# Performance work log

Measured on AMD Instinct MI355X. Metric: run time of the kernel, lower is better.

## Reference

```python
import jax, jax.numpy as jnp
import numpy as np

B, C, L = 16, 384, 4096
KS, NS = 32, 6
KLEN = KS * 2 ** (NS - 1)  # 1024, must be < L
DECAY = 2.0  # multiplier = linspace(2,2,C) == 2 everywhere
EPS = 1e-5


def setup_inputs() -> dict:
    key = jax.random.key(0)
    ks = jax.random.split(key, 10)
    x = jax.random.normal(ks[0], (B, C, L), jnp.float32)
    t_cond = jax.random.normal(ks[1], (B, C // 3, L), jnp.float32)
    # SLConv params (heads=1): per-scale kernels (NS, heads=1, C, KS) and skip D (1, C)
    kernels = jax.random.normal(ks[2], (NS, 1, C, KS), jnp.float32)
    D = jax.random.normal(ks[3], (1, C), jnp.float32)
    # adaLN linear: Linear(C//3 -> 6C). Original zero-inits (identity block); use small random.
    ada_w = jax.random.normal(ks[4], (6 * C, C // 3), jnp.float32) * 0.02
    ada_b = jax.random.normal(ks[5], (6 * C,), jnp.float32) * 0.02
    # 1x1 conv MLP params (kernel_size=1 -> pointwise linear), torch Conv1d init
    lim = 1.0 / np.sqrt(C)
    w1 = jax.random.uniform(ks[6], (C, C), jnp.float32, -lim, lim)
    b1 = jax.random.uniform(ks[7], (C,), jnp.float32, -lim, lim)
    w2 = jax.random.uniform(ks[8], (C, C), jnp.float32, -lim, lim)
    b2 = jax.random.uniform(ks[9], (C,), jnp.float32, -lim, lim)
    return {"x": x, "t_cond": t_cond, "kernels": kernels, "D": D,
            "ada_w": ada_w, "ada_b": ada_b, "w1": w1, "b1": b1, "w2": w2, "b2": b2}


def _channel_ln(x):
    # LayerNorm over channel dim of (B, C, L), no affine (torch eps=1e-5, biased var)
    mu = jnp.mean(x, axis=1, keepdims=True)
    var = jnp.var(x, axis=1, keepdims=True)
    return (x - mu) / jnp.sqrt(var + EPS)


def _slconv(x, kernels, D):
    # Build multi-scale kernel: nearest interp by 2**max(0,i-1), decay multiplier 2**(NS-i-1)
    klist = [jnp.repeat(kernels[i], 2 ** max(0, i - 1), axis=-1) * (DECAY ** (NS - i - 1))
             for i in range(NS)]
    k = jnp.concatenate(klist, axis=-1)  # (1, C, KLEN)
    # first-forward kernel_norm initialization: detached norm
    knorm = jax.lax.stop_gradient(jnp.linalg.norm(k, axis=-1, keepdims=True))
    k = k / knorm
    # FFT conv; SLConv hardcodes padding_mode='constant' -> factor 2
    n = 2 * L
    k_f = jnp.fft.rfft(k, n=n)          # (1, C, n//2+1)
    u_f = jnp.fft.rfft(x, n=n)          # (B, C, n//2+1)
    y_f = u_f[:, None] * k_f[None]      # einsum 'bhl,chl->bchl', heads c=1 -> (B,1,C,n//2+1)
    y = jnp.fft.irfft(y_f, n=n)         # (B, 1, C, 2L)
    ss = KLEN // 2
    y = y[..., ss:ss + L]
    y = y.reshape(B, C, L)              # 'b c h l -> b (h c) l' with heads c=1
    # skip term: einsum('bhl,ch->bchl', x, D) with c=1 collapses to x * D[0]
    return y + x * D[0][None, :, None]


def reference(x, t_cond, kernels, D, ada_w, ada_b, w1, b1, w2, b2):
    y = _channel_ln(x)
    # adaLN: SiLU then Linear over channel dim of t_cond
    t = jax.nn.silu(jnp.swapaxes(t_cond, 1, 2))              # (B, L, C//3)
    temp = jnp.swapaxes(t @ ada_w.T + ada_b, 1, 2)           # (B, 6C, L)
    shift_tm, scale_tm, gate_tm, shift_cm, scale_cm, gate_cm = jnp.split(temp, 6, axis=1)
    y = y * (1.0 + scale_tm) + shift_tm                      # modulate
    y = _slconv(y, kernels, D)
    x = x + gate_tm * y
    y = _channel_ln(x)
    y = y * (1.0 + scale_cm) + shift_cm
    h = jax.nn.gelu(jnp.einsum('oc,bcl->bol', w1, y) + b1[None, :, None], approximate=False)
    m = jnp.einsum('oc,bcl->bol', w2, h) + b2[None, :, None]
    return x + gate_cm * m
```

## Files before the change

kernel.cpp:

```cpp
#include <hip/hip_runtime.h>
#include <cstddef>
#include <cstdint>


namespace {

constexpr int B_  = 16;
constexpr int C_  = 384;
constexpr int L_  = 4096;
constexpr int KADA = 128;
constexpr int KS  = 32;
constexpr int NB  = 6 * 33;
constexpr float EPS_ = 1e-5f;
constexpr int RSA = 136;

typedef unsigned short u16;
typedef __attribute__((ext_vector_type(8))) short bf16x8;
typedef __attribute__((ext_vector_type(4))) float f32x4;
typedef __attribute__((ext_vector_type(4))) float f4;

__device__ __forceinline__ float4 ld4(const float* p) { return *reinterpret_cast<const float4*>(p); }
__device__ __forceinline__ void st4(float* p, float4 v) { *reinterpret_cast<float4*>(p) = v; }
__device__ __forceinline__ float siluf(float z) { return z / (1.f + expf(-z)); }
__device__ __forceinline__ float geluf(float z) { return 0.5f * z * (1.f + erff(z * 0.70710678118654752f)); }
__device__ __forceinline__ u16 f2b(float x) {
  union { float f; uint32_t u; } a; a.f = x;
  const uint32_t u = a.u;
  return (u16)((u + 0x7fffu + ((u >> 16) & 1u)) >> 16);
}
__device__ __forceinline__ float b2f(u16 h) {
  union { uint32_t u; float f; } a; a.u = ((uint32_t)h) << 16; return a.f;
}
__device__ __forceinline__ bf16x8 ldb8(const u16* p) { return *reinterpret_cast<const bf16x8*>(p); }
__device__ __forceinline__ void stb8(u16* p, bf16x8 v) { *reinterpret_cast<bf16x8*>(p) = v; }

__global__ __launch_bounds__(64) void k_kw(const float* __restrict__ kern, float* __restrict__ wb) {
  const int c = blockIdx.x;
  const int t = threadIdx.x;
  constexpr float SC[6] = {32.f, 16.f, 8.f, 4.f, 2.f, 1.f};
  constexpr int REP[6] = {1, 1, 2, 4, 8, 16};
  float part = 0.f;
  for (int idx = t; idx < 192; idx += 64) {
    const int i = idx >> 5, r = idx & 31;
    const float v = kern[(i * C_ + c) * KS + r] * SC[i];
    part += v * v * (float)REP[i];
  }
  for (int m = 1; m < 64; m <<= 1) part += __shfl_xor(part, m);
  const float rinv = 1.f / sqrtf(part);
  for (int jj = t; jj < NB; jj += 64) {
    const int i = jj / 33, r = jj - 33 * i;
    const float sc = SC[i] * rinv;
    float bwv;
    if (r == 0) bwv = kern[(i * C_ + c) * KS + 0] * sc;
    else if (r == 32) bwv = -kern[(i * C_ + c) * KS + 31] * sc;
    else bwv = (kern[(i * C_ + c) * KS + r] - kern[(i * C_ + c) * KS + r - 1]) * sc;
    wb[c * NB + jj] = bwv;
  }
}

__global__ __launch_bounds__(256) void k_wcvt(const float* __restrict__ src, u16* __restrict__ dst) {
  const size_t i = ((size_t)blockIdx.x * 256 + threadIdx.x) * 8;
  const float4 a = ld4(src + i);
  const float4 b = ld4(src + i + 4);
  bf16x8 v;
  v[0] = (short)f2b(a.x); v[1] = (short)f2b(a.y); v[2] = (short)f2b(a.z); v[3] = (short)f2b(a.w);
  v[4] = (short)f2b(b.x); v[5] = (short)f2b(b.y); v[6] = (short)f2b(b.z); v[7] = (short)f2b(b.w);
  stb8(dst + i, v);
}

__global__ __launch_bounds__(256) void k_tsilu(const float* __restrict__ in, u16* __restrict__ out) {
  __shared__ float T[64][65];
  const int t = threadIdx.x;
  const int lb = blockIdx.x * 64;
  const int kb = blockIdx.y * 64;
  const int b  = blockIdx.z;
  const float* src = in + ((size_t)b * KADA + kb) * L_ + lb;
  const int ll = t & 63;
  const int kq = t >> 6;
  #pragma unroll
  for (int j = 0; j < 16; ++j) {
    const int k = kq * 16 + j;
    T[k][ll] = siluf(src[(size_t)k * L_ + ll]);
  }
  __syncthreads();
  const int g = t & 7;
  #pragma unroll
  for (int j = 0; j < 2; ++j) {
    const int l = (t >> 3) + 32 * j;
    bf16x8 v;
    #pragma unroll
    for (int i = 0; i < 8; ++i) v[i] = (short)f2b(T[8 * g + i][l]);
    stb8(out + ((size_t)b * L_ + lb + l) * KADA + kb + 8 * g, v);
  }
}

__global__ __launch_bounds__(256) void k_mv4(const float* __restrict__ x,
                                             float* __restrict__ mu, float* __restrict__ rs) {
  const int g4 = blockIdx.x * 256 + threadIdx.x;
  const int b = g4 >> 10;
  const int l = (g4 & 1023) * 4;
  const float* p = x + (size_t)b * C_ * L_ + l;
  f4 s = {0.f, 0.f, 0.f, 0.f}, ss = {0.f, 0.f, 0.f, 0.f};
  #pragma unroll 4
  for (int c = 0; c < C_; ++c) {
    const f4 v = *reinterpret_cast<const f4*>(p + (size_t)c * L_);
    s += v; ss += v * v;
  }
  f4 m4, r4;
  #pragma unroll
  for (int e = 0; e < 4; ++e) {
    const float m = s[e] * (1.f / (float)C_);
    const float var = ss[e] * (1.f / (float)C_) - m * m;
    m4[e] = m;
    r4[e] = 1.f / sqrtf(var + EPS_);
  }
  *reinterpret_cast<f4*>(mu + (size_t)b * L_ + l) = m4;
  *reinterpret_cast<f4*>(rs + (size_t)b * L_ + l) = r4;
}

template <int KD, int NBOP>
__device__ __forceinline__ void gemm_core3(const u16* __restrict__ Ab,
                                           const u16* __restrict__ B0b,
                                           const u16* __restrict__ B1b,
                                           u16* As, u16* Bs,
                                           f32x4 (&acc0)[4][4], f32x4 (&acc1)[4][4]) {
  constexpr int WC = (NBOP == 2) ? 2 : 4;
  const int tid = threadIdx.x;
  const int lane = tid & 63;
  const int wid = tid >> 6;
  const int wl = (wid & 1) * 64;
  const int wc = (wid >> 1) * ((NBOP == 2) ? 32 : 64);
  const int frow = lane & 15;
  const int fk8 = (lane >> 4) * 8;
  const int rr = tid >> 4;
  const int c8 = (tid & 15) * 8;

  for (int kc = 0; kc < KD; kc += 128) {
    __syncthreads();
    #pragma unroll
    for (int j = 0; j < 8; ++j)
      stb8(As + (j * 16 + rr) * RSA + c8, ldb8(Ab + (size_t)(j * 16 + rr) * KD + kc + c8));
    #pragma unroll
    for (int j = 0; j < 4; ++j)
      stb8(Bs + (j * 16 + rr) * RSA + c8, ldb8(B0b + (size_t)(j * 16 + rr) * KD + kc + c8));
    #pragma unroll
    for (int j = 0; j < 4; ++j)
      stb8(Bs + ((j + 4) * 16 + rr) * RSA + c8, ldb8(B1b + (size_t)(j * 16 + rr) * KD + kc + c8));
    __syncthreads();
    #pragma unroll
    for (int ks = 0; ks < 128; ks += 32) {
      bf16x8 af[4], b0f[WC], b1f[WC];
      #pragma unroll
      for (int fi = 0; fi < 4; ++fi)
        af[fi] = ldb8(As + (wl + fi * 16 + frow) * RSA + ks + fk8);
      #pragma unroll
      for (int fj = 0; fj < WC; ++fj) {
        b0f[fj] = ldb8(Bs + (wc + fj * 16 + frow) * RSA + ks + fk8);
        if constexpr (NBOP == 2)
          b1f[fj] = ldb8(Bs + (64 + wc + fj * 16 + frow) * RSA + ks + fk8);
      }
      #pragma unroll
      for (int fi = 0; fi < 4; ++fi)
        #pragma unroll
        for (int fj = 0; fj < WC; ++fj) {
          acc0[fi][fj] = __builtin_amdgcn_mfma_f32_16x16x32_bf16(af[fi], b0f[fj], acc0[fi][fj], 0, 0, 0);
          if constexpr (NBOP == 2)
            acc1[fi][fj] = __builtin_amdgcn_mfma_f32_16x16x32_bf16(af[fi], b1f[fj], acc1[fi][fj], 0, 0, 0);
        }
    }
  }
}

template <int MODE>
__global__ __launch_bounds__(256) void k_adagemm(const u16* __restrict__ AWB,
                                                 const float* __restrict__ ada_b,
                                                 const u16* __restrict__ STT,
                                                 const float* __restrict__ src,
                                                 const float* __restrict__ mu,
                                                 const float* __restrict__ rs,
                                                 float* __restrict__ dstf,
                                                 u16* __restrict__ dstb,
                                                 int base0, int base1) {
  __shared__ u16 As[128 * RSA];
  __shared__ u16 Bs[128 * RSA];
  const int lb = blockIdx.x * 128;
  const int b  = blockIdx.z;
  f32x4 acc0[4][4] = {};
  f32x4 acc1[4][4] = {};
  constexpr int NBOP = (MODE == 2) ? 1 : 2;
  const int cb = blockIdx.y * ((MODE == 2) ? 128 : 64);
  const u16* B0b;
  const u16* B1b;
  if constexpr (MODE == 2) {
    B0b = AWB + (size_t)(base0 + cb) * KADA;
    B1b = AWB + (size_t)(base0 + cb + 64) * KADA;
  } else {
    B0b = AWB + (size_t)(base0 + cb) * KADA;
    B1b = AWB + (size_t)(base1 + cb) * KADA;
  }
  gemm_core3<KADA, NBOP>(STT + ((size_t)b * L_ + lb) * KADA, B0b, B1b, As, Bs, acc0, acc1);

  const int lane = threadIdx.x & 63;
  const int wid = threadIdx.x >> 6;
  const int wl = (wid & 1) * 64;
  const int wc = (wid >> 1) * ((NBOP == 2) ? 32 : 64);
  const int frow = lane & 15;
  const int fq = (lane >> 4) * 4;
  constexpr int WC = (NBOP == 2) ? 2 : 4;
  #pragma unroll
  for (int fi = 0; fi < 4; ++fi) {
    const int lg = lb + wl + fi * 16 + fq;
    float4 m4, r4;
    if (MODE != 2) { m4 = ld4(mu + (size_t)b * L_ + lg); r4 = ld4(rs + (size_t)b * L_ + lg); }
    #pragma unroll
    for (int fj = 0; fj < WC; ++fj) {
      const int cg = cb + wc + fj * 16 + frow;
      const size_t n = ((size_t)b * C_ + cg) * L_ + lg;
      if (MODE == 2) {
        const float bg = ada_b[base0 + cg];
        const u16 h0 = f2b(acc0[fi][fj][0] + bg);
        const u16 h1 = f2b(acc0[fi][fj][1] + bg);
        const u16 h2 = f2b(acc0[fi][fj][2] + bg);
        const u16 h3 = f2b(acc0[fi][fj][3] + bg);
        uint2 pk;
        pk.x = (uint32_t)h0 | ((uint32_t)h1 << 16);
        pk.y = (uint32_t)h2 | ((uint32_t)h3 << 16);
        *reinterpret_cast<uint2*>(dstb + n) = pk;
      } else {
        const float bsh = ada_b[base0 + cg];
        const float bsc = ada_b[base1 + cg];
        const float4 xv = ld4(src + n);
        float o[4];
        o[0] = (xv.x - m4.x) * r4.x * (1.f + acc1[fi][fj][0] + bsc) + acc0[fi][fj][0] + bsh;
        o[1] = (xv.y - m4.y) * r4.y * (1.f + acc1[fi][fj][1] + bsc) + acc0[fi][fj][1] + bsh;
        o[2] = (xv.z - m4.z) * r4.z * (1.f + acc1[fi][fj][2] + bsc) + acc0[fi][fj][2] + bsh;
        o[3] = (xv.w - m4.w) * r4.w * (1.f + acc1[fi][fj][3] + bsc) + acc0[fi][fj][3] + bsh;
        if (MODE == 0) {
          st4(dstf + n, float4{o[0], o[1], o[2], o[3]});
        } else {
          u16* d = dstb + ((size_t)b * L_ + lg) * C_ + cg;
          #pragma unroll
          for (int i = 0; i < 4; ++i) d[(size_t)i * C_] = f2b(o[i]);
        }
      }
    }
  }
}

__global__ __launch_bounds__(256) void k_mlp1(const u16* __restrict__ Y3T,
                                              const u16* __restrict__ W1B,
                                              const float* __restrict__ b1,
                                              u16* __restrict__ HT) {
  __shared__ u16 As[128 * RSA];
  __shared__ u16 Bs[128 * RSA];
  const int lb = blockIdx.x * 128;
  const int cb = blockIdx.y * 128;
  const int b  = blockIdx.z;
  f32x4 acc0[4][4] = {};
  f32x4 accd[4][4];
  gemm_core3<C_, 1>(Y3T + ((size_t)b * L_ + lb) * C_,
                    W1B + (size_t)cb * C_, W1B + (size_t)(cb + 64) * C_,
                    As, Bs, acc0, accd);
  const int lane = threadIdx.x & 63;
  const int wid = threadIdx.x >> 6;
  const int wl = (wid & 1) * 64;
  const int wc = (wid >> 1) * 64;
  const int frow = lane & 15;
  const int fq = (lane >> 4) * 4;
  #pragma unroll
  for (int fi = 0; fi < 4; ++fi) {
    const int lg = lb + wl + fi * 16 + fq;
    #pragma unroll
    for (int fj = 0; fj < 4; ++fj) {
      const int hg = cb + wc + fj * 16 + frow;
      const float bo = b1[hg];
      u16* d = HT + ((size_t)b * L_ + lg) * C_ + hg;
      #pragma unroll
      for (int i = 0; i < 4; ++i) d[(size_t)i * C_] = f2b(geluf(acc0[fi][fj][i] + bo));
    }
  }
}

__global__ __launch_bounds__(256) void k_final(const u16* __restrict__ HT,
                                               const u16* __restrict__ W2B,
                                               const float* __restrict__ b2,
                                               const u16* __restrict__ AWB,
                                               const float* __restrict__ ada_b,
                                               const u16* __restrict__ STT,
                                               float* __restrict__ out,
                                               int gbase) {
  __shared__ u16 As[128 * RSA];
  __shared__ u16 Bs[128 * RSA];
  const int lb = blockIdx.x * 128;
  const int cb = blockIdx.y * 128;
  const int b  = blockIdx.z;
  f32x4 accM[4][4] = {};
  f32x4 accG[4][4] = {};
  f32x4 accd[4][4];
  gemm_core3<C_, 1>(HT + ((size_t)b * L_ + lb) * C_,
                    W2B + (size_t)cb * C_, W2B + (size_t)(cb + 64) * C_,
                    As, Bs, accM, accd);
  gemm_core3<KADA, 1>(STT + ((size_t)b * L_ + lb) * KADA,
                      AWB + (size_t)(gbase + cb) * KADA,
                      AWB + (size_t)(gbase + cb + 64) * KADA,
                      As, Bs, accG, accd);
  const int lane = threadIdx.x & 63;
  const int wid = threadIdx.x >> 6;
  const int wl = (wid & 1) * 64;
  const int wc = (wid >> 1) * 64;
  const int frow = lane & 15;
  const int fq = (lane >> 4) * 4;
  #pragma unroll
  for (int fi = 0; fi < 4; ++fi) {
    const int lg = lb + wl + fi * 16 + fq;
    #pragma unroll
    for (int fj = 0; fj < 4; ++fj) {
      const int cg = cb + wc + fj * 16 + frow;
      const float bo = b2[cg];
      const float bg = ada_b[gbase + cg];
      const size_t n = ((size_t)b * C_ + cg) * L_ + lg;
      const float4 xv = ld4(out + n);
      float4 o;
      o.x = xv.x + (accG[fi][fj][0] + bg) * (accM[fi][fj][0] + bo);
      o.y = xv.y + (accG[fi][fj][1] + bg) * (accM[fi][fj][1] + bo);
      o.z = xv.z + (accG[fi][fj][2] + bg) * (accM[fi][fj][2] + bo);
      o.w = xv.w + (accG[fi][fj][3] + bg) * (accM[fi][fj][3] + bo);
      st4(out + n, o);
    }
  }
}

__device__ __forceinline__ int swz(int q) { return q ^ ((q >> 3) & 7); }

__device__ __forceinline__ float wf5(const f4& W0, const f4& W1, const f4& W2,
                                     const f4& W3, const f4& W4, int j) {
  return j < 4 ? W0[j & 3] : j < 8 ? W1[j & 3] : j < 12 ? W2[j & 3]
       : j < 16 ? W3[j & 3] : W4[j & 3];
}
__device__ __forceinline__ float wf4(const f4& W0, const f4& W1, const f4& W2,
                                     const f4& W3, int j) {
  return j < 4 ? W0[j & 3] : j < 8 ? W1[j & 3] : j < 12 ? W2[j & 3] : W3[j & 3];
}

__global__ __launch_bounds__(256) void k_convfused(const float* __restrict__ Ymod,
                                                   const float* __restrict__ x,
                                                   const u16* __restrict__ G,
                                                   const float* __restrict__ wb,
                                                   const float* __restrict__ Dv,
                                                   float* __restrict__ out) {
  __shared__ f4 Q4s[1280];
  __shared__ float aux[256];
  const int tid = threadIdx.x;
  const int c = blockIdx.x % C_;
  const size_t rowoff = (size_t)blockIdx.x * L_;

  f4 v[4];
  {
    const float* yrow = Ymod + rowoff;
    #pragma unroll
    for (int j = 0; j < 4; ++j)
      v[j] = *reinterpret_cast<const f4*>(yrow + 16 * tid + 4 * j);
    float run = 0.f;
    #pragma unroll
    for (int j = 0; j < 4; ++j) {
      v[j][0] += run; v[j][1] += v[j][0]; v[j][2] += v[j][1]; v[j][3] += v[j][2];
      run = v[j][3];
    }
    aux[tid] = run;
  }
  __syncthreads();
  for (int off = 1; off < 256; off <<= 1) {
    const float t = (tid >= off) ? aux[tid - off] : 0.f;
    __syncthreads();
    aux[tid] += t;
    __syncthreads();
  }
  const float excl = tid ? aux[tid - 1] : 0.f;
  const float total = aux[255];
  #pragma unroll
  for (int j = 0; j < 4; ++j) {
    v[j][0] += excl; v[j][1] += excl; v[j][2] += excl; v[j][3] += excl;
    Q4s[swz(128 + 4 * tid + j)] = v[j];
  }
  if (tid < 128) {
    Q4s[swz(tid)] = f4{0.f, 0.f, 0.f, 0.f};
    Q4s[swz(1152 + tid)] = f4{total, total, total, total};
  }
  __syncthreads();

  const float* wrow = wb + c * NB;
  const int qb = 256 + 4 * tid;
  float acc[16];
  #pragma unroll
  for (int i = 0; i < 16; ++i) acc[i] = 0.f;

  #pragma unroll
  for (int s = 0; s < 2; ++s) {
    const int wbase = s * 33;
    const int q0 = qb - 1 - 8 * s;
    float w[33];
    #pragma unroll
    for (int r = 0; r < 33; ++r) w[r] = wrow[wbase + r];
    f4 W0 = Q4s[swz(q0)],     W1 = Q4s[swz(q0 + 1)], W2 = Q4s[swz(q0 + 2)],
       W3 = Q4s[swz(q0 + 3)], W4 = Q4s[swz(q0 + 4)];
    #pragma unroll
    for (int g = 0; g < 9; ++g) {
      #pragma unroll
      for (int d = 0; d < 4; ++d) {
        if (g < 8 || d == 0) {
          #pragma unroll
          for (int i = 0; i < 16; ++i)
            acc[i] += w[4 * g + d] * wf5(W0, W1, W2, W3, W4, i + 4 - d);
        }
      }
      if (g < 8) { W4 = W3; W3 = W2; W2 = W1; W1 = W0; W0 = Q4s[swz(q0 - 1 - g)]; }
    }
  }
  {
    const int q0 = qb - 17;
    float w[33];
    #pragma unroll
    for (int r = 0; r < 33; ++r) w[r] = wrow[66 + r];
    f4 W0 = Q4s[swz(q0)],     W1 = Q4s[swz(q0 + 1)], W2 = Q4s[swz(q0 + 2)],
       W3 = Q4s[swz(q0 + 3)], W4 = Q4s[swz(q0 + 4)];
    #pragma unroll
    for (int h = 0; h < 17; ++h) {
      #pragma unroll
      for (int i = 0; i < 16; ++i)
        acc[i] += w[2 * h] * wf5(W0, W1, W2, W3, W4, i + 4);
      if (h < 16) {
        #pragma unroll
        for (int i = 0; i < 16; ++i)
          acc[i] += w[2 * h + 1] * wf5(W0, W1, W2, W3, W4, i + 2);
        W4 = W3; W3 = W2; W2 = W1; W1 = W0; W0 = Q4s[swz(q0 - 1 - h)];
      }
    }
  }
  {
    const int low0 = qb - 32;
    float w[33];
    #pragma unroll
    for (int r = 0; r < 33; ++r) w[r] = wrow[99 + r];
    f4 W0 = Q4s[swz(low0)],     W1 = Q4s[swz(low0 + 1)],
       W2 = Q4s[swz(low0 + 2)], W3 = Q4s[swz(low0 + 3)];
    #pragma unroll
    for (int r = 0; r < 33; ++r) {
      #pragma unroll
      for (int i = 0; i < 16; ++i) acc[i] += w[r] * wf4(W0, W1, W2, W3, i);
      if (r < 32) { W3 = W2; W2 = W1; W1 = W0; W0 = Q4s[swz(low0 - 1 - r)]; }
    }
  }
  {
    const int low0 = qb - 64;
    float w[33];
    #pragma unroll
    for (int r = 0; r < 33; ++r) w[r] = wrow[132 + r];
    f4 W0 = Q4s[swz(low0)],     W1 = Q4s[swz(low0 + 1)],
       W2 = Q4s[swz(low0 + 2)], W3 = Q4s[swz(low0 + 3)];
    #pragma unroll
    for (int r = 0; r < 33; ++r) {
      #pragma unroll
      for (int i = 0; i < 16; ++i) acc[i] += w[r] * wf4(W0, W1, W2, W3, i);
      if (r < 32) {
        W3 = W1; W2 = W0;
        W0 = Q4s[swz(low0 - 2 * r - 2)];
        W1 = Q4s[swz(low0 - 2 * r - 1)];
      }
    }
  }
  {
    float w[33];
    #pragma unroll
    for (int r = 0; r < 33; ++r) w[r] = wrow[165 + r];
    #pragma unroll
    for (int r = 0; r < 33; ++r) {
      const int lo = qb - 128 - 4 * r;
      const f4 W0 = Q4s[swz(lo)],     W1 = Q4s[swz(lo + 1)],
               W2 = Q4s[swz(lo + 2)], W3 = Q4s[swz(lo + 3)];
      #pragma unroll
      for (int i = 0; i < 16; ++i) acc[i] += w[r] * wf4(W0, W1, W2, W3, i);
    }
  }

  const float Dc = Dv[c];
  const float* xrow = x + rowoff + 16 * tid;
  const u16* grow = G + rowoff + 16 * tid;
  float* orow = out + rowoff + 16 * tid;
  const bf16x8 g0 = ldb8(grow);
  const bf16x8 g1 = ldb8(grow + 8);
  float pprev = excl;
  #pragma unroll
  for (int a = 0; a < 4; ++a) {
    const f4 xv = *reinterpret_cast<const f4*>(xrow + 4 * a);
    f4 o;
    #pragma unroll
    for (int e = 0; e < 4; ++e) {
      const int i = 4 * a + e;
      const float y2 = acc[i] + (v[a][e] - pprev) * Dc;
      const float gv = b2f((u16)(i < 8 ? g0[i] : g1[i - 8]));
      o[e] = xv[e] + gv * y2;
      pprev = v[a][e];
    }
    *reinterpret_cast<f4*>(orow + 4 * a) = o;
  }
}

}

extern "C" void kernel_launch(void* const* d_in, const int* in_sizes, int n_in,
                              void* d_out, int out_size, void* d_ws, size_t ws_size,
                              hipStream_t stream) {
  const float* x      = (const float*)d_in[0];
  const float* t_cond = (const float*)d_in[1];
  const float* kern   = (const float*)d_in[2];
  const float* Dv     = (const float*)d_in[3];
  const float* ada_w  = (const float*)d_in[4];
  const float* ada_b  = (const float*)d_in[5];
  const float* w1     = (const float*)d_in[6];
  const float* b1     = (const float*)d_in[7];
  const float* w2     = (const float*)d_in[8];
  const float* b2     = (const float*)d_in[9];
  float* out = (float*)d_out;

  float* wsf = (float*)d_ws;
  float* A  = wsf;
  float* MV = A + (size_t)B_ * C_ * L_;
  float* WB = MV + 4 * (size_t)B_ * L_;
  u16* AWB = (u16*)(WB + (size_t)C_ * NB);
  u16* W1B = AWB + (size_t)6 * C_ * KADA;
  u16* W2B = W1B + (size_t)C_ * C_;
  u16* STT = W2B + (size_t)C_ * C_;
  u16* Y3T = STT + (size_t)B_ * L_ * KADA;
  u16* HT  = Y3T + (size_t)B_ * L_ * C_;
  u16* G   = Y3T;
  float* mu1 = MV;
  float* rs1 = MV + (size_t)B_ * L_;
  float* mu2 = MV + 2 * (size_t)B_ * L_;
  float* rs2 = MV + 3 * (size_t)B_ * L_;

  (void)in_sizes; (void)n_in; (void)out_size; (void)ws_size;

  const dim3 gg2(L_ / 128, 6, B_);
  const dim3 gg3(L_ / 128, 3, B_);

  k_kw<<<C_, 64, 0, stream>>>(kern, WB);
  k_wcvt<<<(6 * C_ * KADA) / 2048, 256, 0, stream>>>(ada_w, AWB);
  k_wcvt<<<(C_ * C_) / 2048, 256, 0, stream>>>(w1, W1B);
  k_wcvt<<<(C_ * C_) / 2048, 256, 0, stream>>>(w2, W2B);
  k_tsilu<<<dim3(L_ / 64, KADA / 64, B_), 256, 0, stream>>>(t_cond, STT);

  k_mv4<<<(B_ * L_ / 4) / 256, 256, 0, stream>>>(x, mu1, rs1);
  k_adagemm<0><<<gg2, 256, 0, stream>>>(AWB, ada_b, STT, x, mu1, rs1, A, nullptr, 0, C_);
  k_adagemm<2><<<gg3, 256, 0, stream>>>(AWB, ada_b, STT, nullptr, nullptr, nullptr, nullptr, G, 2 * C_, 0);
  k_convfused<<<B_ * C_, 256, 0, stream>>>(A, x, G, WB, Dv, out);
  k_mv4<<<(B_ * L_ / 4) / 256, 256, 0, stream>>>(out, mu2, rs2);
  k_adagemm<1><<<gg2, 256, 0, stream>>>(AWB, ada_b, STT, out, mu2, rs2, nullptr, Y3T, 3 * C_, 4 * C_);
  k_mlp1<<<gg3, 256, 0, stream>>>(Y3T, W1B, b1, HT);
  k_final<<<gg3, 256, 0, stream>>>(HT, W2B, b2, AWB, ada_b, STT, out, 5 * C_);
}
```

Measured before the change: 647.6 us.

## Move row prefix-sum totals into adaLN GEMM epilogue and drop block scan

The modulate GEMM epilogue now computes per-128-column partial sums for each (batch, channel) row. A small new kernel scans these into per-segment offsets and a row total. The conv kernel then replaces its 256-step LDS Hillis-Steele scan, with its many barriers, by a width-8 shuffle scan plus the precomputed offsets. The skip-term differences are rebuilt from the LDS prefix array. This adds one tiny launch plus extra shared-memory reduction and barriers in the GEMM epilogue, in exchange for shorter conv-kernel synchronisation.

```diff
diff --git a/kernel.cpp b/kernel.cpp
--- a/kernel.cpp
+++ b/kernel.cpp
@@ -180,6 +180,7 @@
                                                  const float* __restrict__ rs,
                                                  float* __restrict__ dstf,
                                                  u16* __restrict__ dstb,
+                                                 float* __restrict__ part,
                                                  int base0, int base1) {
   __shared__ u16 As[128 * RSA];
   __shared__ u16 Bs[128 * RSA];
@@ -207,6 +208,7 @@
   const int frow = lane & 15;
   const int fq = (lane >> 4) * 4;
   constexpr int WC = (NBOP == 2) ? 2 : 4;
+  float csum[2] = {0.f, 0.f};
   #pragma unroll
   for (int fi = 0; fi < 4; ++fi) {
     const int lg = lb + wl + fi * 16 + fq;
@@ -237,6 +239,7 @@
         o[3] = (xv.w - m4.w) * r4.w * (1.f + acc1[fi][fj][3] + bsc) + acc0[fi][fj][3] + bsh;
         if (MODE == 0) {
           st4(dstf + n, float4{o[0], o[1], o[2], o[3]});
+          csum[fj] += (o[0] + o[1]) + (o[2] + o[3]);
         } else {
           u16* d = dstb + ((size_t)b * L_ + lg) * C_ + cg;
           #pragma unroll
@@ -245,6 +248,38 @@
       }
     }
   }
+  if constexpr (MODE == 0) {
+    __syncthreads();
+    float* S = reinterpret_cast<float*>(As);
+    #pragma unroll
+    for (int fj = 0; fj < 2; ++fj) {
+      float v = csum[fj];
+      v += __shfl_xor(v, 16);
+      v += __shfl_xor(v, 32);
+      if (lane < 16) S[(wid & 1) * 64 + wc + fj * 16 + frow] = v;
+    }
+    __syncthreads();
+    if (threadIdx.x < 64) {
+      const int cg = cb + threadIdx.x;
+      part[((size_t)b * C_ + cg) * 32 + blockIdx.x] = S[threadIdx.x] + S[64 + threadIdx.x];
+    }
+  }
+}
+
+__global__ __launch_bounds__(256) void k_off(const float* __restrict__ part,
+                                             float* __restrict__ off) {
+  const int tid = threadIdx.x;
+  const int row = blockIdx.x * 8 + (tid >> 5);
+  const int j = tid & 31;
+  const float v = part[(size_t)row * 32 + j];
+  float incl = v;
+  #pragma unroll
+  for (int d = 1; d < 32; d <<= 1) {
+    const float t = __shfl_up(incl, d, 32);
+    if (j >= d) incl += t;
+  }
+  off[(size_t)row * 33 + j] = incl - v;
+  if (j == 31) off[(size_t)row * 33 + 32] = incl;
 }
 
 __global__ __launch_bounds__(256) void k_mlp1(const u16* __restrict__ Y3T,
@@ -342,49 +377,47 @@
   return j < 4 ? W0[j & 3] : j < 8 ? W1[j & 3] : j < 12 ? W2[j & 3] : W3[j & 3];
 }
 
-__global__ __launch_bounds__(256) void k_convfused(const float* __restrict__ Ymod,
-                                                   const float* __restrict__ x,
-                                                   const u16* __restrict__ G,
-                                                   const float* __restrict__ wb,
-                                                   const float* __restrict__ Dv,
-                                                   float* __restrict__ out) {
+__global__ __launch_bounds__(256) void k_convG(const float* __restrict__ Ymod,
+                                               const float* __restrict__ x,
+                                               const u16* __restrict__ G,
+                                               const float* __restrict__ Off,
+                                               const float* __restrict__ wb,
+                                               const float* __restrict__ Dv,
+                                               float* __restrict__ out) {
   __shared__ f4 Q4s[1280];
-  __shared__ float aux[256];
   const int tid = threadIdx.x;
   const int c = blockIdx.x % C_;
   const size_t rowoff = (size_t)blockIdx.x * L_;
-
-  f4 v[4];
+  const float* offrow = Off + (size_t)blockIdx.x * 33;
+
   {
-    const float* yrow = Ymod + rowoff;
-    #pragma unroll
-    for (int j = 0; j < 4; ++j)
-      v[j] = *reinterpret_cast<const f4*>(yrow + 16 * tid + 4 * j);
+    const float* yrow = Ymod + rowoff + 16 * tid;
+    f4 v[4];
+    #pragma unroll
+    for (int j = 0; j < 4; ++j) v[j] = *reinterpret_cast<const f4*>(yrow + 4 * j);
     float run = 0.f;
     #pragma unroll
     for (int j = 0; j < 4; ++j) {
       v[j][0] += run; v[j][1] += v[j][0]; v[j][2] += v[j][1]; v[j][3] += v[j][2];
       run = v[j][3];
     }
-    aux[tid] = run;
-  }
-  __syncthreads();
-  for (int off = 1; off < 256; off <<= 1) {
-    const float t = (tid >= off) ? aux[tid - off] : 0.f;
-    __syncthreads();
-    aux[tid] += t;
-    __syncthreads();
-  }
-  const float excl = tid ? aux[tid - 1] : 0.f;
-  const float total = aux[255];
-  #pragma unroll
-  for (int j = 0; j < 4; ++j) {
-    v[j][0] += excl; v[j][1] += excl; v[j][2] += excl; v[j][3] += excl;
-    Q4s[swz(128 + 4 * tid + j)] = v[j];
-  }
-  if (tid < 128) {
-    Q4s[swz(tid)] = f4{0.f, 0.f, 0.f, 0.f};
-    Q4s[swz(1152 + tid)] = f4{total, total, total, total};
+    float incl = run;
+    #pragma unroll
+    for (int d = 1; d < 8; d <<= 1) {
+      const float t = __shfl_up(incl, d, 8);
+      if ((tid & 7) >= d) incl += t;
+    }
+    const float base = offrow[tid >> 3] + (incl - run);
+    #pragma unroll
+    for (int j = 0; j < 4; ++j) {
+      v[j][0] += base; v[j][1] += base; v[j][2] += base; v[j][3] += base;
+      Q4s[swz(128 + 4 * tid + j)] = v[j];
+    }
+    const float total = offrow[32];
+    if (tid < 128) {
+      Q4s[swz(tid)] = f4{0.f, 0.f, 0.f, 0.f};
+      Q4s[swz(1152 + tid)] = f4{total, total, total, total};
+    }
   }
   __syncthreads();
 
@@ -483,12 +516,17 @@
   }
 
   const float Dc = Dv[c];
+  const int qe = 128 + 4 * tid;
+  const f4 E0 = Q4s[swz(qe - 1)], E1 = Q4s[swz(qe)],     E2 = Q4s[swz(qe + 1)],
+           E3 = Q4s[swz(qe + 2)], E4 = Q4s[swz(qe + 3)];
+  float pm[17];
+  #pragma unroll
+  for (int j = 0; j < 17; ++j) pm[j] = wf5(E0, E1, E2, E3, E4, j + 3);
   const float* xrow = x + rowoff + 16 * tid;
   const u16* grow = G + rowoff + 16 * tid;
   float* orow = out + rowoff + 16 * tid;
   const bf16x8 g0 = ldb8(grow);
   const bf16x8 g1 = ldb8(grow + 8);
-  float pprev = excl;
   #pragma unroll
   for (int a = 0; a < 4; ++a) {
     const f4 xv = *reinterpret_cast<const f4*>(xrow + 4 * a);
@@ -496,10 +534,9 @@
     #pragma unroll
     for (int e = 0; e < 4; ++e) {
       const int i = 4 * a + e;
-      const float y2 = acc[i] + (v[a][e] - pprev) * Dc;
+      const float y2 = acc[i] + (pm[i + 1] - pm[i]) * Dc;
       const float gv = b2f((u16)(i < 8 ? g0[i] : g1[i - 8]));
       o[e] = xv[e] + gv * y2;
-      pprev = v[a][e];
     }
     *reinterpret_cast<f4*>(orow + 4 * a) = o;
   }
@@ -523,10 +560,12 @@
   float* out = (float*)d_out;
 
   float* wsf = (float*)d_ws;
-  float* A  = wsf;
-  float* MV = A + (size_t)B_ * C_ * L_;
-  float* WB = MV + 4 * (size_t)B_ * L_;
-  u16* AWB = (u16*)(WB + (size_t)C_ * NB);
+  float* A    = wsf;
+  float* MV   = A + (size_t)B_ * C_ * L_;
+  float* WB   = MV + 4 * (size_t)B_ * L_;
+  float* Part = WB + (size_t)C_ * NB;
+  float* Off  = Part + (size_t)B_ * C_ * 32;
+  u16* AWB = (u16*)(Off + (size_t)B_ * C_ * 33);
   u16* W1B = AWB + (size_t)6 * C_ * KADA;
   u16* W2B = W1B + (size_t)C_ * C_;
   u16* STT = W2B + (size_t)C_ * C_;
@@ -550,11 +589,12 @@
   k_tsilu<<<dim3(L_ / 64, KADA / 64, B_), 256, 0, stream>>>(t_cond, STT);
 
   k_mv4<<<(B_ * L_ / 4) / 256, 256, 0, stream>>>(x, mu1, rs1);
-  k_adagemm<0><<<gg2, 256, 0, stream>>>(AWB, ada_b, STT, x, mu1, rs1, A, nullptr, 0, C_);
-  k_adagemm<2><<<gg3, 256, 0, stream>>>(AWB, ada_b, STT, nullptr, nullptr, nullptr, nullptr, G, 2 * C_, 0);
-  k_convfused<<<B_ * C_, 256, 0, stream>>>(A, x, G, WB, Dv, out);
+  k_adagemm<0><<<gg2, 256, 0, stream>>>(AWB, ada_b, STT, x, mu1, rs1, A, nullptr, Part, 0, C_);
+  k_off<<<(B_ * C_) / 8, 256, 0, stream>>>(Part, Off);
+  k_adagemm<2><<<gg3, 256, 0, stream>>>(AWB, ada_b, STT, nullptr, nullptr, nullptr, nullptr, G, nullptr, 2 * C_, 0);
+  k_convG<<<B_ * C_, 256, 0, stream>>>(A, x, G, Off, WB, Dv, out);
   k_mv4<<<(B_ * L_ / 4) / 256, 256, 0, stream>>>(out, mu2, rs2);
-  k_adagemm<1><<<gg2, 256, 0, stream>>>(AWB, ada_b, STT, out, mu2, rs2, nullptr, Y3T, 3 * C_, 4 * C_);
+  k_adagemm<1><<<gg2, 256, 0, stream>>>(AWB, ada_b, STT, out, mu2, rs2, nullptr, Y3T, nullptr, 3 * C_, 4 * C_);
   k_mlp1<<<gg3, 256, 0, stream>>>(Y3T, W1B, b1, HT);
   k_final<<<gg3, 256, 0, stream>>>(HT, W2B, b2, AWB, ada_b, STT, out, 5 * C_);
 }
```

New measurement: 531.3 us, median of 3. -18.0%, faster.

## Rewrite fused long conv as single-wavefront blocks with 64 outputs per thread

Applied to the files above, without the earlier changes.

The prefix-sum based multi-scale convolution kernel is restructured so each block is one 64-thread wavefront and each thread computes 64 consecutive outputs. The block-wide scan through shared memory with many barriers becomes a wave-level shuffle scan. The per-scale loops now keep a 16 to 17 entry register window over the prefix array, which is meant to raise data reuse per LDS read. The D skip term is folded into the accumulator initialisation. In exchange each thread holds far more registers and blocks are much smaller, which risks lower occupancy and less latency hiding.

```diff
diff --git a/kernel.cpp b/kernel.cpp
--- a/kernel.cpp
+++ b/kernel.cpp
@@ -330,178 +330,216 @@
   }
 }
 
-__device__ __forceinline__ int swz(int q) { return q ^ ((q >> 3) & 7); }
-
-__device__ __forceinline__ float wf5(const f4& W0, const f4& W1, const f4& W2,
-                                     const f4& W3, const f4& W4, int j) {
-  return j < 4 ? W0[j & 3] : j < 8 ? W1[j & 3] : j < 12 ? W2[j & 3]
-       : j < 16 ? W3[j & 3] : W4[j & 3];
-}
-__device__ __forceinline__ float wf4(const f4& W0, const f4& W1, const f4& W2,
-                                     const f4& W3, int j) {
-  return j < 4 ? W0[j & 3] : j < 8 ? W1[j & 3] : j < 12 ? W2[j & 3] : W3[j & 3];
-}
-
-__global__ __launch_bounds__(256) void k_convfused(const float* __restrict__ Ymod,
-                                                   const float* __restrict__ x,
-                                                   const u16* __restrict__ G,
-                                                   const float* __restrict__ wb,
-                                                   const float* __restrict__ Dv,
-                                                   float* __restrict__ out) {
+__device__ __forceinline__ int z16(int q) { return q ^ ((q >> 4) & 7); }
+
+__global__ __launch_bounds__(64, 2) void k_convG2(const float* __restrict__ Ymod,
+                                                  const float* __restrict__ x,
+                                                  const u16* __restrict__ G,
+                                                  const float* __restrict__ wb,
+                                                  const float* __restrict__ Dv,
+                                                  float* __restrict__ out) {
   __shared__ f4 Q4s[1280];
-  __shared__ float aux[256];
-  const int tid = threadIdx.x;
+  const int t = threadIdx.x;
   const int c = blockIdx.x % C_;
   const size_t rowoff = (size_t)blockIdx.x * L_;
-
-  f4 v[4];
-  {
-    const float* yrow = Ymod + rowoff;
-    #pragma unroll
-    for (int j = 0; j < 4; ++j)
-      v[j] = *reinterpret_cast<const f4*>(yrow + 16 * tid + 4 * j);
+  const float Dc = Dv[c];
+
+  f4 acc[16];
+  {
+    const float* yrow = Ymod + rowoff + 64 * t;
+    f4 y[16];
+    #pragma unroll
+    for (int j = 0; j < 16; ++j) y[j] = *reinterpret_cast<const f4*>(yrow + 4 * j);
+    #pragma unroll
+    for (int g = 0; g < 16; ++g) acc[g] = y[g] * Dc;
     float run = 0.f;
     #pragma unroll
-    for (int j = 0; j < 4; ++j) {
-      v[j][0] += run; v[j][1] += v[j][0]; v[j][2] += v[j][1]; v[j][3] += v[j][2];
-      run = v[j][3];
-    }
-    aux[tid] = run;
+    for (int j = 0; j < 16; ++j) {
+      y[j][0] += run; y[j][1] += y[j][0]; y[j][2] += y[j][1]; y[j][3] += y[j][2];
+      run = y[j][3];
+    }
+    float incl = run;
+    #pragma unroll
+    for (int d = 1; d < 64; d <<= 1) {
+      const float tv = __shfl_up(incl, d, 64);
+      if (t >= d) incl += tv;
+    }
+    const float base = incl - run;
+    const float total = __shfl(incl, 63, 64);
+    #pragma unroll
+    for (int j = 0; j < 16; ++j) {
+      f4 vv = y[j];
+      vv[0] += base; vv[1] += base; vv[2] += base; vv[3] += base;
+      Q4s[z16(128 + 16 * t + j)] = vv;
+    }
+    Q4s[z16(t)] = f4{0.f, 0.f, 0.f, 0.f};
+    Q4s[z16(64 + t)] = f4{0.f, 0.f, 0.f, 0.f};
+    Q4s[z16(1152 + t)] = f4{total, total, total, total};
+    Q4s[z16(1216 + t)] = f4{total, total, total, total};
   }
   __syncthreads();
-  for (int off = 1; off < 256; off <<= 1) {
-    const float t = (tid >= off) ? aux[tid - off] : 0.f;
-    __syncthreads();
-    aux[tid] += t;
-    __syncthreads();
-  }
-  const float excl = tid ? aux[tid - 1] : 0.f;
-  const float total = aux[255];
-  #pragma unroll
-  for (int j = 0; j < 4; ++j) {
-    v[j][0] += excl; v[j][1] += excl; v[j][2] += excl; v[j][3] += excl;
-    Q4s[swz(128 + 4 * tid + j)] = v[j];
-  }
-  if (tid < 128) {
-    Q4s[swz(tid)] = f4{0.f, 0.f, 0.f, 0.f};
-    Q4s[swz(1152 + tid)] = f4{total, total, total, total};
-  }
-  __syncthreads();
 
   const float* wrow = wb + c * NB;
-  const int qb = 256 + 4 * tid;
-  float acc[16];
-  #pragma unroll
-  for (int i = 0; i < 16; ++i) acc[i] = 0.f;
-
-  #pragma unroll
-  for (int s = 0; s < 2; ++s) {
-    const int wbase = s * 33;
-    const int q0 = qb - 1 - 8 * s;
-    float w[33];
-    #pragma unroll
-    for (int r = 0; r < 33; ++r) w[r] = wrow[wbase + r];
-    f4 W0 = Q4s[swz(q0)],     W1 = Q4s[swz(q0 + 1)], W2 = Q4s[swz(q0 + 2)],
-       W3 = Q4s[swz(q0 + 3)], W4 = Q4s[swz(q0 + 4)];
-    #pragma unroll
-    for (int g = 0; g < 9; ++g) {
-      #pragma unroll
-      for (int d = 0; d < 4; ++d) {
-        if (g < 8 || d == 0) {
+
+  {
+    f4 W[16];
+    #pragma unroll
+    for (int g = 0; g < 16; ++g) W[g] = Q4s[z16(16 * t + g)];
+    for (int kb = 0; kb < 8; ++kb) {
+      #pragma unroll
+      for (int u = 0; u < 4; ++u) {
+        const int k = 4 * kb + u;
+        const float wr = wrow[197 - k];
+        #pragma unroll
+        for (int g = 0; g < 16; ++g) acc[g] += wr * W[(g + 4 * u) & 15];
+        #pragma unroll
+        for (int d = 0; d < 4; ++d)
+          W[(4 * u + d) & 15] = Q4s[z16(16 * t + 16 + 4 * k + d)];
+      }
+    }
+    const float wr = wrow[165];
+    #pragma unroll
+    for (int g = 0; g < 16; ++g) acc[g] += wr * W[g];
+  }
+
+  {
+    f4 W[16];
+    #pragma unroll
+    for (int g = 0; g < 16; ++g) W[g] = Q4s[z16(128 + 16 * t + g)];
+    for (int kb = 0; kb < 4; ++kb) {
+      #pragma unroll
+      for (int u = 0; u < 8; ++u) {
+        const int k = 8 * kb + u;
+        const float wr = wrow[164 - k];
+        #pragma unroll
+        for (int g = 0; g < 16; ++g) acc[g] += wr * W[(g + 2 * u) & 15];
+        #pragma unroll
+        for (int d = 0; d < 2; ++d)
+          W[(2 * u + d) & 15] = Q4s[z16(128 + 16 * t + 16 + 2 * k + d)];
+      }
+    }
+    const float wr = wrow[132];
+    #pragma unroll
+    for (int g = 0; g < 16; ++g) acc[g] += wr * W[g];
+  }
+
+  {
+    f4 W[16];
+    #pragma unroll
+    for (int g = 0; g < 16; ++g) W[g] = Q4s[z16(192 + 16 * t + g)];
+    for (int kb = 0; kb < 2; ++kb) {
+      #pragma unroll
+      for (int u = 0; u < 16; ++u) {
+        const int k = 16 * kb + u;
+        const float wr = wrow[131 - k];
+        #pragma unroll
+        for (int g = 0; g < 16; ++g) acc[g] += wr * W[(g + u) & 15];
+        W[u] = Q4s[z16(192 + 16 * t + 16 + k)];
+      }
+    }
+    const float wr = wrow[99];
+    #pragma unroll
+    for (int g = 0; g < 16; ++g) acc[g] += wr * W[g];
+  }
+
+  {
+    f4 W[17];
+    #pragma unroll
+    for (int j = 0; j < 17; ++j) W[j] = Q4s[z16(223 + 16 * t + j)];
+    {
+      const float we = wrow[66 + 32];
+      #pragma unroll
+      for (int g = 0; g < 16; ++g) acc[g] += we * W[1 + g];
+    }
+    for (int h = 15; h >= 0; --h) {
+      #pragma unroll
+      for (int j = 0; j < 16; ++j) W[j] = W[j + 1];
+      W[16] = Q4s[z16(255 + 16 * t - h)];
+      const float we = wrow[66 + 2 * h];
+      const float wo = wrow[66 + 2 * h + 1];
+      #pragma unroll
+      for (int g = 0; g < 16; ++g) {
+        acc[g] += we * W[1 + g];
+        acc[g][0] += wo * W[g][2];
+        acc[g][1] += wo * W[g][3];
+        acc[g][2] += wo * W[1 + g][0];
+        acc[g][3] += wo * W[1 + g][1];
+      }
+    }
+  }
+
+  {
+    f4 W[17];
+    #pragma unroll
+    for (int j = 0; j < 17; ++j) W[j] = Q4s[z16(239 + 16 * t + j)];
+    {
+      const float w0 = wrow[33 + 32];
+      #pragma unroll
+      for (int g = 0; g < 16; ++g) acc[g] += w0 * W[1 + g];
+    }
+    for (int s = 7; s >= 0; --s) {
+      #pragma unroll
+      for (int j = 0; j < 16; ++j) W[j] = W[j + 1];
+      W[16] = Q4s[z16(263 + 16 * t - s)];
+      #pragma unroll
+      for (int u = 0; u < 4; ++u) {
+        const float wr = wrow[33 + 4 * s + u];
+        #pragma unroll
+        for (int g = 0; g < 16; ++g) {
           #pragma unroll
-          for (int i = 0; i < 16; ++i)
-            acc[i] += w[4 * g + d] * wf5(W0, W1, W2, W3, W4, i + 4 - d);
+          for (int e = 0; e < 4; ++e) {
+            const float pv = (e >= u) ? W[1 + g][e - u] : W[g][4 + e - u];
+            acc[g][e] += wr * pv;
+          }
         }
       }
-      if (g < 8) { W4 = W3; W3 = W2; W2 = W1; W1 = W0; W0 = Q4s[swz(q0 - 1 - g)]; }
-    }
-  }
-  {
-    const int q0 = qb - 17;
-    float w[33];
-    #pragma unroll
-    for (int r = 0; r < 33; ++r) w[r] = wrow[66 + r];
-    f4 W0 = Q4s[swz(q0)],     W1 = Q4s[swz(q0 + 1)], W2 = Q4s[swz(q0 + 2)],
-       W3 = Q4s[swz(q0 + 3)], W4 = Q4s[swz(q0 + 4)];
-    #pragma unroll
-    for (int h = 0; h < 17; ++h) {
-      #pragma unroll
-      for (int i = 0; i < 16; ++i)
-        acc[i] += w[2 * h] * wf5(W0, W1, W2, W3, W4, i + 4);
-      if (h < 16) {
-        #pragma unroll
-        for (int i = 0; i < 16; ++i)
-          acc[i] += w[2 * h + 1] * wf5(W0, W1, W2, W3, W4, i + 2);
-        W4 = W3; W3 = W2; W2 = W1; W1 = W0; W0 = Q4s[swz(q0 - 1 - h)];
-      }
-    }
-  }
-  {
-    const int low0 = qb - 32;
-    float w[33];
-    #pragma unroll
-    for (int r = 0; r < 33; ++r) w[r] = wrow[99 + r];
-    f4 W0 = Q4s[swz(low0)],     W1 = Q4s[swz(low0 + 1)],
-       W2 = Q4s[swz(low0 + 2)], W3 = Q4s[swz(low0 + 3)];
-    #pragma unroll
-    for (int r = 0; r < 33; ++r) {
-      #pragma unroll
-      for (int i = 0; i < 16; ++i) acc[i] += w[r] * wf4(W0, W1, W2, W3, i);
-      if (r < 32) { W3 = W2; W2 = W1; W1 = W0; W0 = Q4s[swz(low0 - 1 - r)]; }
-    }
-  }
-  {
-    const int low0 = qb - 64;
-    float w[33];
-    #pragma unroll
-    for (int r = 0; r < 33; ++r) w[r] = wrow[132 + r];
-    f4 W0 = Q4s[swz(low0)],     W1 = Q4s[swz(low0 + 1)],
-       W2 = Q4s[swz(low0 + 2)], W3 = Q4s[swz(low0 + 3)];
-    #pragma unroll
-    for (int r = 0; r < 33; ++r) {
-      #pragma unroll
-      for (int i = 0; i < 16; ++i) acc[i] += w[r] * wf4(W0, W1, W2, W3, i);
-      if (r < 32) {
-        W3 = W1; W2 = W0;
-        W0 = Q4s[swz(low0 - 2 * r - 2)];
-        W1 = Q4s[swz(low0 - 2 * r - 1)];
-      }
-    }
-  }
-  {
-    float w[33];
-    #pragma unroll
-    for (int r = 0; r < 33; ++r) w[r] = wrow[165 + r];
-    #pragma unroll
-    for (int r = 0; r < 33; ++r) {
-      const int lo = qb - 128 - 4 * r;
-      const f4 W0 = Q4s[swz(lo)],     W1 = Q4s[swz(lo + 1)],
-               W2 = Q4s[swz(lo + 2)], W3 = Q4s[swz(lo + 3)];
-      #pragma unroll
-      for (int i = 0; i < 16; ++i) acc[i] += w[r] * wf4(W0, W1, W2, W3, i);
-    }
-  }
-
-  const float Dc = Dv[c];
-  const float* xrow = x + rowoff + 16 * tid;
-  const u16* grow = G + rowoff + 16 * tid;
-  float* orow = out + rowoff + 16 * tid;
-  const bf16x8 g0 = ldb8(grow);
-  const bf16x8 g1 = ldb8(grow + 8);
-  float pprev = excl;
-  #pragma unroll
-  for (int a = 0; a < 4; ++a) {
-    const f4 xv = *reinterpret_cast<const f4*>(xrow + 4 * a);
-    f4 o;
-    #pragma unroll
-    for (int e = 0; e < 4; ++e) {
-      const int i = 4 * a + e;
-      const float y2 = acc[i] + (v[a][e] - pprev) * Dc;
-      const float gv = b2f((u16)(i < 8 ? g0[i] : g1[i - 8]));
-      o[e] = xv[e] + gv * y2;
-      pprev = v[a][e];
-    }
-    *reinterpret_cast<f4*>(orow + 4 * a) = o;
+    }
+  }
+
+  {
+    f4 W[17];
+    #pragma unroll
+    for (int j = 0; j < 17; ++j) W[j] = Q4s[z16(247 + 16 * t + j)];
+    {
+      const float w0 = wrow[32];
+      #pragma unroll
+      for (int g = 0; g < 16; ++g) acc[g] += w0 * W[1 + g];
+    }
+    for (int s = 7; s >= 0; --s) {
+      #pragma unroll
+      for (int j = 0; j < 16; ++j) W[j] = W[j + 1];
+      W[16] = Q4s[z16(271 + 16 * t - s)];
+      #pragma unroll
+      for (int u = 0; u < 4; ++u) {
+        const float wr = wrow[4 * s + u];
+        #pragma unroll
+        for (int g = 0; g < 16; ++g) {
+          #pragma unroll
+          for (int e = 0; e < 4; ++e) {
+            const float pv = (e >= u) ? W[1 + g][e - u] : W[g][4 + e - u];
+            acc[g][e] += wr * pv;
+          }
+        }
+      }
+    }
+  }
+
+  const float* xrow = x + rowoff + 64 * t;
+  const u16*  grow = G + rowoff + 64 * t;
+  float* orow = out + rowoff + 64 * t;
+  #pragma unroll
+  for (int a = 0; a < 8; ++a) {
+    const bf16x8 gv = ldb8(grow + 8 * a);
+    #pragma unroll
+    for (int half = 0; half < 2; ++half) {
+      const int g = 2 * a + half;
+      const f4 xv = *reinterpret_cast<const f4*>(xrow + 8 * a + 4 * half);
+      f4 o;
+      #pragma unroll
+      for (int e = 0; e < 4; ++e)
+        o[e] = xv[e] + b2f((u16)gv[4 * half + e]) * acc[g][e];
+      *reinterpret_cast<f4*>(orow + 8 * a + 4 * half) = o;
+    }
   }
 }
 
@@ -523,9 +561,9 @@
   float* out = (float*)d_out;
 
   float* wsf = (float*)d_ws;
-  float* A  = wsf;
-  float* MV = A + (size_t)B_ * C_ * L_;
-  float* WB = MV + 4 * (size_t)B_ * L_;
+  float* A    = wsf;
+  float* MV   = A + (size_t)B_ * C_ * L_;
+  float* WB   = MV + 4 * (size_t)B_ * L_;
   u16* AWB = (u16*)(WB + (size_t)C_ * NB);
   u16* W1B = AWB + (size_t)6 * C_ * KADA;
   u16* W2B = W1B + (size_t)C_ * C_;
@@ -552,7 +590,7 @@
   k_mv4<<<(B_ * L_ / 4) / 256, 256, 0, stream>>>(x, mu1, rs1);
   k_adagemm<0><<<gg2, 256, 0, stream>>>(AWB, ada_b, STT, x, mu1, rs1, A, nullptr, 0, C_);
   k_adagemm<2><<<gg3, 256, 0, stream>>>(AWB, ada_b, STT, nullptr, nullptr, nullptr, nullptr, G, 2 * C_, 0);
-  k_convfused<<<B_ * C_, 256, 0, stream>>>(A, x, G, WB, Dv, out);
+  k_convG2<<<B_ * C_, 64, 0, stream>>>(A, x, G, WB, Dv, out);
   k_mv4<<<(B_ * L_ / 4) / 256, 256, 0, stream>>>(out, mu2, rs2);
   k_adagemm<1><<<gg2, 256, 0, stream>>>(AWB, ada_b, STT, out, mu2, rs2, nullptr, Y3T, 3 * C_, 4 * C_);
   k_mlp1<<<gg3, 256, 0, stream>>>(Y3T, W1B, b1, HT);
```

New measurement: 553.5 us. 14.5% less time.
